# Performance work log

Measured on AMD Instinct MI355X. Metric: run time of the kernel, lower is better.

Reference implementation:

```python
import jax, jax.numpy as jnp
import numpy as np

NUM_NODES = 100000
NUM_EDGES = 500000
HID = 256


def setup_inputs() -> dict:
    key = jax.random.key(0)
    ks = jax.random.split(key, 6)
    emb_src = jax.random.normal(ks[0], (NUM_NODES, HID), dtype=jnp.float32)
    emb_dst = jax.random.normal(ks[1], (NUM_NODES, HID), dtype=jnp.float32)
    edge_label_index = jax.random.randint(ks[2], (2, NUM_EDGES), 0, NUM_NODES, dtype=jnp.int32)
    # torch Linear(2H, H) weight is [H, 2H]; we store transposed [2H, H] for x @ W
    W1 = jax.random.normal(ks[3], (2 * HID, HID), dtype=jnp.float32) * (1.0 / np.sqrt(2 * HID))
    b1 = jnp.zeros((HID,), dtype=jnp.float32)
    W2 = jax.random.normal(ks[4], (HID, 1), dtype=jnp.float32) * (1.0 / np.sqrt(HID))
    b2 = jnp.zeros((1,), dtype=jnp.float32)
    return {"emb_src": emb_src, "emb_dst": emb_dst, "edge_label_index": edge_label_index,
            "W1": W1, "b1": b1, "W2": W2, "b2": b2}


def reference(emb_src, emb_dst, edge_label_index, W1, b1, W2, b2):
    # decode(): gather src/dst embeddings, concat, Linear-ReLU-Linear, squeeze
    src_idx = edge_label_index[0]
    dst_idx = edge_label_index[1]
    h_src = emb_src[src_idx]          # [E, H] irregular gather
    h_dst = emb_dst[dst_idx]          # [E, H]
    # concat([h_src, h_dst]) @ W1 == h_src @ W1[:H] + h_dst @ W1[H:]
    # (avoids materializing the [E, 2H] concatenated tensor)
    h = jnp.dot(h_src, W1[:HID]) + jnp.dot(h_dst, W1[HID:]) + b1  # [E, H]
    h = jax.nn.relu(h)
    logits = (jnp.dot(h, W2) + b2)[:, 0]  # [E]
    return logits
```

## Files before the change

kernel.cpp:

```cpp
#include <hip/hip_runtime.h>
#include <hip/hip_bf16.h>
#include <stdint.h>

#define HID 256
#define BM  64
#define LDA 68
#define LDC 264

typedef __bf16 bf16x8 __attribute__((ext_vector_type(8)));
typedef float  f32x4  __attribute__((ext_vector_type(4)));

__device__ __forceinline__ ushort f2bf(float x) {
    union { float f; uint32_t u; } v; v.f = x;
    uint32_t u = v.u;
    uint32_t r = u + 0x7fffu + ((u >> 16) & 1u);
    return (ushort)(r >> 16);
}

__device__ __forceinline__ uint32_t pack2bf(float a, float b) {
    union { float f; uint32_t u; } ua, ub;
    ua.f = a; ub.f = b;
    return __builtin_amdgcn_perm(ub.u + 0x8000u, ua.u + 0x8000u, 0x07060302u);
}

__device__ __forceinline__ float uaf(uint32_t x) {
    union { uint32_t u; float f; } c; c.u = x; return c.f;
}

__global__ void conv_w1(const float* __restrict__ W1, ushort* __restrict__ Wt4) {
    __shared__ ushort tr[32][33];
    const int bk = blockIdx.x >> 3;
    const int bn = blockIdx.x & 7;
    const int t  = threadIdx.x;
    #pragma unroll
    for (int i = 0; i < 4; ++i) {
        int e = t + 256 * i; int r = e >> 5, cc = e & 31;
        tr[cc][r] = f2bf(W1[(size_t)(bk * 32 + r) * HID + bn * 32 + cc]);
    }
    __syncthreads();
    #pragma unroll
    for (int i = 0; i < 4; ++i) {
        int e = t + 256 * i; int rn = e >> 5, ck = e & 31;
        int k = bk * 32 + ck;
        int grp = k >> 3;
        int j   = k & 7;
        int n   = bn * 32 + rn;
        Wt4[((size_t)grp * HID + n) * 8 + j] = tr[rn][ck];
    }
}

__global__ __launch_bounds__(256, 4)
void node_gemm(const float* __restrict__ emb0, const float* __restrict__ emb1,
               const ushort* __restrict__ Wt4,
               ushort* __restrict__ u0, ushort* __restrict__ u1,
               int n0, int n1, int nb0) {
    __shared__ __align__(16) union {
        ushort As[4][BM * LDA];
        ushort Cs[32 * LDC];
    } sm;

    const int t    = threadIdx.x;
    const int tb   = (blockIdx.x >= nb0) ? 1 : 0;
    const int bloc = blockIdx.x - tb * nb0;
    const float*  emb = tb ? emb1 : emb0;
    ushort*       uo  = tb ? u1 : u0;
    const int     n   = tb ? n1 : n0;
    const int     e0  = bloc * BM;

    const int wave = t >> 6, lane = t & 63, q = lane >> 4, cl = lane & 15;

    const int r0  = t >> 4, seg = t & 15;
    int rcl[4];
    #pragma unroll
    for (int i = 0; i < 4; ++i) {
        int r = e0 + r0 + 16 * i; if (r > n - 1) r = n - 1;
        rcl[i] = r;
    }
    const float* abase = emb + seg * 4;
    const int    sbase = r0 * LDA + seg * 4;

    {
        float4 g[4][4];
        #pragma unroll
        for (int c = 0; c < 4; ++c)
            #pragma unroll
            for (int i = 0; i < 4; ++i)
                g[c][i] = *reinterpret_cast<const float4*>(
                    abase + (size_t)rcl[i] * HID + c * 64);
        #pragma unroll
        for (int c = 0; c < 4; ++c)
            #pragma unroll
            for (int i = 0; i < 4; ++i) {
                uint2 v;
                v.x = pack2bf(g[c][i].x, g[c][i].y);
                v.y = pack2bf(g[c][i].z, g[c][i].w);
                *reinterpret_cast<uint2*>(&sm.As[c][sbase + i * 16 * LDA]) = v;
            }
    }
    __syncthreads();

    f32x4 acc[4][4] = {};

    #pragma unroll 1
    for (int c = 0; c < 4; ++c) {
        bf16x8 bfr[2][4];
        #pragma unroll
        for (int ks = 0; ks < 2; ++ks) {
            const ushort* bb = Wt4 + ((size_t)(tb * 32 + c * 8 + ks * 4 + q) * HID) * 8;
            #pragma unroll
            for (int ni = 0; ni < 4; ++ni)
                bfr[ks][ni] = *reinterpret_cast<const bf16x8*>(
                    bb + (wave * 64 + ni * 16 + cl) * 8);
        }
        #pragma unroll
        for (int ks = 0; ks < 2; ++ks) {
            bf16x8 af[4];
            #pragma unroll
            for (int mi = 0; mi < 4; ++mi)
                af[mi] = *reinterpret_cast<const bf16x8*>(
                    &sm.As[c][(mi * 16 + cl) * LDA + ks * 32 + q * 8]);
            #pragma unroll
            for (int mi = 0; mi < 4; ++mi)
                #pragma unroll
                for (int ni = 0; ni < 4; ++ni)
                    acc[mi][ni] = __builtin_amdgcn_mfma_f32_16x16x32_bf16(
                        af[mi], bfr[ks][ni], acc[mi][ni], 0, 0, 0);
        }
    }

    __syncthreads();

    #pragma unroll
    for (int h = 0; h < 2; ++h) {
        #pragma unroll
        for (int mh = 0; mh < 2; ++mh) {
            const int mi = h * 2 + mh;
            #pragma unroll
            for (int ni = 0; ni < 4; ++ni)
                #pragma unroll
                for (int r = 0; r < 4; ++r)
                    sm.Cs[(mh * 16 + q * 4 + r) * LDC + wave * 64 + ni * 16 + cl] =
                        f2bf(acc[mi][ni][r]);
        }
        __syncthreads();

        #pragma unroll
        for (int i = 0; i < 4; ++i) {
            int f = t + 256 * i;
            int row = f >> 5, unit = f & 31;
            int grow = e0 + h * 32 + row;
            if (grow < n) {
                uint4 w = *reinterpret_cast<const uint4*>(&sm.Cs[row * LDC + unit * 8]);
                *reinterpret_cast<uint4*>(uo + (size_t)grow * HID + unit * 8) = w;
            }
        }
        if (h == 0) __syncthreads();
    }
}

#define EB 8
__global__ __launch_bounds__(256, 4)
void lp_edge(const ushort* __restrict__ u, const ushort* __restrict__ v,
             const int* __restrict__ eli,
             const float* __restrict__ b1, const float* __restrict__ W2,
             const float* __restrict__ b2, float* __restrict__ out,
             int E, int nwaves) {
    const int lane = threadIdx.x & 63;
    const int half = lane >> 5, sub = lane & 31;
    const int wid  = blockIdx.x * (blockDim.x >> 6) + (threadIdx.x >> 6);

    float b1v[8], w2v[8];
    {
        const float4* p1 = reinterpret_cast<const float4*>(b1 + sub * 8);
        const float4* p2 = reinterpret_cast<const float4*>(W2 + sub * 8);
        float4 a = p1[0], b = p1[1], c = p2[0], d = p2[1];
        b1v[0]=a.x; b1v[1]=a.y; b1v[2]=a.z; b1v[3]=a.w;
        b1v[4]=b.x; b1v[5]=b.y; b1v[6]=b.z; b1v[7]=b.w;
        w2v[0]=c.x; w2v[1]=c.y; w2v[2]=c.z; w2v[3]=c.w;
        w2v[4]=d.x; w2v[5]=d.y; w2v[6]=d.z; w2v[7]=d.w;
    }
    const float bias2 = b2[0];
    const ushort* tab  = half ? v : u;
    const int*    idxp = eli + (size_t)half * E;

    auto gather = [&](int b, uint4* gg) {
        #pragma unroll
        for (int j = 0; j < EB; ++j) {
            int e = b + j; if (e > E - 1) e = E - 1;
            int row = idxp[e];
            gg[j] = *reinterpret_cast<const uint4*>(tab + (size_t)row * HID + sub * 8);
        }
    };
    auto process = [&](const uint4* gg, int b) {
        float res = 0.f;
        #pragma unroll
        for (int j = 0; j < EB; ++j) {
            uint32_t pd[4], gd[4] = { gg[j].x, gg[j].y, gg[j].z, gg[j].w };
            #pragma unroll
            for (int c = 0; c < 4; ++c) pd[c] = (uint32_t)__shfl_xor((int)gd[c], 32);
            float acc = 0.f;
            #pragma unroll
            for (int c = 0; c < 4; ++c) {
                float a0 = uaf(gd[c] << 16), a1 = uaf(gd[c] & 0xffff0000u);
                float o0 = uaf(pd[c] << 16), o1 = uaf(pd[c] & 0xffff0000u);
                float h0 = fmaxf(a0 + o0 + b1v[2 * c], 0.f);
                float h1 = fmaxf(a1 + o1 + b1v[2 * c + 1], 0.f);
                acc = fmaf(h0, w2v[2 * c], acc);
                acc = fmaf(h1, w2v[2 * c + 1], acc);
            }
            #pragma unroll
            for (int m = 1; m <= 16; m <<= 1) acc += __shfl_xor(acc, m);
            if (half == 0 && sub == j) res = acc + bias2;
        }
        int e = b + sub;
        if (half == 0 && sub < EB && e < E) out[e] = res;
    };

    const int step = nwaves * EB;
    int base = wid * EB;
    uint4 gA[EB], gB[EB];
    gather(base, gA);
    while (base < E) {
        gather(base + step, gB);
        process(gA, base);
        base += step;
        if (base >= E) break;
        gather(base + step, gA);
        process(gB, base);
        base += step;
    }
}

__global__ __launch_bounds__(256, 3)
void lp_mono(const float* __restrict__ es, const float* __restrict__ ed,
             const int* __restrict__ eli, const float* __restrict__ W1,
             const float* __restrict__ b1, const float* __restrict__ W2,
             const float* __restrict__ b2,
             float* __restrict__ out, int E) {
    __shared__ __align__(16) ushort As[2][BM * LDA];
    __shared__ int   sIdx[2][BM];
    __shared__ float hred[4][BM];

    const int t = threadIdx.x, e0 = blockIdx.x * BM;
    const int wave = t >> 6, lane = t & 63, q = lane >> 4, cl = lane & 15;

    if (t < 2 * BM) {
        int which = t >> 6, e = t & 63;
        int ge = e0 + e; if (ge > E - 1) ge = E - 1;
        sIdx[which][e] = eli[which * E + ge];
    }
    __syncthreads();

    int ge_[2], go_[2], rsrc[2], rdst[2];
    #pragma unroll
    for (int i = 0; i < 2; ++i) {
        int c2 = t + 256 * i;
        ge_[i] = c2 >> 3; go_[i] = c2 & 7;
        rsrc[i] = sIdx[0][ge_[i]];
        rdst[i] = sIdx[1][ge_[i]];
    }
    float4 g0[2], g1[2];
    auto gather = [&](int c) {
        const float* tab = (c < 4) ? es : ed;
        #pragma unroll
        for (int i = 0; i < 2; ++i) {
            int row = (c < 4) ? rsrc[i] : rdst[i];
            const float* p = tab + (size_t)row * HID + (c & 3) * 64 + go_[i] * 8;
            g0[i] = *reinterpret_cast<const float4*>(p);
            g1[i] = *reinterpret_cast<const float4*>(p + 4);
        }
    };
    auto cvstore = [&](int buf) {
        #pragma unroll
        for (int i = 0; i < 2; ++i) {
            uint4 v;
            v.x = pack2bf(g0[i].x, g0[i].y); v.y = pack2bf(g0[i].z, g0[i].w);
            v.z = pack2bf(g1[i].x, g1[i].y); v.w = pack2bf(g1[i].z, g1[i].w);
            *reinterpret_cast<uint4*>(&As[buf][ge_[i] * LDA + go_[i] * 8]) = v;
        }
    };
    gather(0); cvstore(0); __syncthreads();
    f32x4 acc[4][4] = {};
    #pragma unroll
    for (int c = 0; c < 8; ++c) {
        const int cur = c & 1;
        if (c < 7) gather(c + 1);
        #pragma unroll
        for (int ks = 0; ks < 2; ++ks) {
            bf16x8 af[4], bfr[4];
            #pragma unroll
            for (int mi = 0; mi < 4; ++mi)
                af[mi] = *reinterpret_cast<const bf16x8*>(
                    &As[cur][(mi * 16 + cl) * LDA + ks * 32 + q * 8]);
            #pragma unroll
            for (int ni = 0; ni < 4; ++ni) {
                int nn = wave * 64 + ni * 16 + cl;
                union { ushort s[8]; bf16x8 v; } u;
                #pragma unroll
                for (int j = 0; j < 8; ++j)
                    u.s[j] = f2bf(W1[(size_t)(c * 64 + ks * 32 + q * 8 + j) * HID + nn]);
                bfr[ni] = u.v;
            }
            #pragma unroll
            for (int mi = 0; mi < 4; ++mi)
                #pragma unroll
                for (int ni = 0; ni < 4; ++ni)
                    acc[mi][ni] = __builtin_amdgcn_mfma_f32_16x16x32_bf16(
                        af[mi], bfr[ni], acc[mi][ni], 0, 0, 0);
        }
        if (c < 7) { cvstore(cur ^ 1); __syncthreads(); }
    }
    float b1v[4], w2v[4];
    #pragma unroll
    for (int ni = 0; ni < 4; ++ni) {
        int col = wave * 64 + ni * 16 + cl;
        b1v[ni] = b1[col]; w2v[ni] = W2[col];
    }
    #pragma unroll
    for (int mi = 0; mi < 4; ++mi) {
        #pragma unroll
        for (int r = 0; r < 4; ++r) {
            float s = 0.f;
            #pragma unroll
            for (int ni = 0; ni < 4; ++ni) {
                float h = acc[mi][ni][r] + b1v[ni];
                h = fmaxf(h, 0.f);
                s += h * w2v[ni];
            }
            s += __shfl_xor(s, 1); s += __shfl_xor(s, 2);
            s += __shfl_xor(s, 4); s += __shfl_xor(s, 8);
            if (cl == 0) hred[wave][mi * 16 + q * 4 + r] = s;
        }
    }
    __syncthreads();
    if (t < BM) {
        int ge = e0 + t;
        if (ge < E)
            out[ge] = hred[0][t] + hred[1][t] + hred[2][t] + hred[3][t] + b2[0];
    }
}

extern "C" void kernel_launch(void* const* d_in, const int* in_sizes, int n_in,
                              void* d_out, int out_size, void* d_ws, size_t ws_size,
                              hipStream_t stream) {
    const float* emb_src = (const float*)d_in[0];
    const float* emb_dst = (const float*)d_in[1];
    const int*   eli     = (const int*)d_in[2];
    const float* W1      = (const float*)d_in[3];
    const float* b1      = (const float*)d_in[4];
    const float* W2      = (const float*)d_in[5];
    const float* b2      = (const float*)d_in[6];
    float*       out     = (float*)d_out;

    const int E   = in_sizes[2] / 2;
    const int n0n = in_sizes[0] / HID;
    const int n1n = in_sizes[1] / HID;

    const size_t wtB = (size_t)2 * HID * 2 * HID * sizeof(ushort);
    const size_t uB  = (size_t)n0n * HID * sizeof(ushort);
    const size_t vB  = (size_t)n1n * HID * sizeof(ushort);

    ushort* Wt4 = (ushort*)d_ws;
    ushort* u0  = (ushort*)((char*)d_ws + wtB);
    ushort* u1  = (ushort*)((char*)d_ws + wtB + uB);

    const int fullPath = ws_size >= wtB + uB + vB;

    if (fullPath) {
        conv_w1<<<128, 256, 0, stream>>>(W1, Wt4);
        const int nb0 = (n0n + BM - 1) / BM;
        const int nb1 = (n1n + BM - 1) / BM;
        node_gemm<<<nb0 + nb1, 256, 0, stream>>>(emb_src, emb_dst, Wt4,
                                                 u0, u1, n0n, n1n, nb0);
        const int eb = 2048;
        lp_edge<<<eb, 256, 0, stream>>>(u0, u1, eli, b1, W2, b2, out, E, eb * 4);
    } else {
        const int nb = (E + BM - 1) / BM;
        lp_mono<<<nb, 256, 0, stream>>>(emb_src, emb_dst, eli, W1,
                                        b1, W2, b2, out, E);
    }
}
```

Baseline: 324.9 us.

## Make node GEMM persistent with double-buffered prefetch of embedding chunks

Turns node_gemm into a persistent kernel on a grid of at most 1024 blocks that loops over tiles. It double-buffers the A tile in LDS by K-chunk, prefetching the next chunk (or the next tile's first chunk) into registers while the MFMAs run on the current one. The LDS-staged coalesced output store is replaced with direct scattered 2-byte global stores from the accumulators. This shrinks shared memory use, but adds a barrier per chunk, uncoalesced output writes and a lower launch-bounds occupancy hint.

```diff
diff --git a/kernel.cpp b/kernel.cpp
--- a/kernel.cpp
+++ b/kernel.cpp
@@ -49,112 +49,132 @@
     }
 }
 
-__global__ __launch_bounds__(256, 4)
+__global__ __launch_bounds__(256, 3)
 void node_gemm(const float* __restrict__ emb0, const float* __restrict__ emb1,
                const ushort* __restrict__ Wt4,
                ushort* __restrict__ u0, ushort* __restrict__ u1,
-               int n0, int n1, int nb0) {
-    __shared__ __align__(16) union {
-        ushort As[4][BM * LDA];
-        ushort Cs[32 * LDC];
-    } sm;
+               int n0, int n1, int nb0, int ntiles) {
+    __shared__ __align__(16) ushort As[2][BM * LDA];
 
     const int t    = threadIdx.x;
-    const int tb   = (blockIdx.x >= nb0) ? 1 : 0;
-    const int bloc = blockIdx.x - tb * nb0;
-    const float*  emb = tb ? emb1 : emb0;
-    ushort*       uo  = tb ? u1 : u0;
-    const int     n   = tb ? n1 : n0;
-    const int     e0  = bloc * BM;
-
     const int wave = t >> 6, lane = t & 63, q = lane >> 4, cl = lane & 15;
-
-    const int r0  = t >> 4, seg = t & 15;
-    int rcl[4];
+    const int r0   = t >> 4, seg = t & 15;
+    const int sbase = r0 * LDA + seg * 4;
+
+    int tile = blockIdx.x;
+    if (tile >= ntiles) return;
+
+    int tbA = (tile >= nb0) ? 1 : 0;
+    const float* embA = tbA ? emb1 : emb0;
+    ushort*      uoA  = tbA ? u1 : u0;
+    int nA  = tbA ? n1 : n0;
+    int e0A = (tile - tbA * nb0) * BM;
+    int rclA[4];
     #pragma unroll
     for (int i = 0; i < 4; ++i) {
-        int r = e0 + r0 + 16 * i; if (r > n - 1) r = n - 1;
-        rcl[i] = r;
-    }
-    const float* abase = emb + seg * 4;
-    const int    sbase = r0 * LDA + seg * 4;
-
-    {
-        float4 g[4][4];
-        #pragma unroll
-        for (int c = 0; c < 4; ++c)
-            #pragma unroll
-            for (int i = 0; i < 4; ++i)
-                g[c][i] = *reinterpret_cast<const float4*>(
-                    abase + (size_t)rcl[i] * HID + c * 64);
-        #pragma unroll
-        for (int c = 0; c < 4; ++c)
+        int r = e0A + r0 + 16 * i; if (r > nA - 1) r = nA - 1;
+        rclA[i] = r;
+    }
+
+    float4 g[4];
+    auto cvstore = [&](int buf) {
+        #pragma unroll
+        for (int i = 0; i < 4; ++i) {
+            uint2 v;
+            v.x = pack2bf(g[i].x, g[i].y);
+            v.y = pack2bf(g[i].z, g[i].w);
+            *reinterpret_cast<uint2*>(&As[buf][sbase + i * 16 * LDA]) = v;
+        }
+    };
+
+    #pragma unroll
+    for (int i = 0; i < 4; ++i)
+        g[i] = *reinterpret_cast<const float4*>(embA + (size_t)rclA[i] * HID + seg * 4);
+    cvstore(0);
+    __syncthreads();
+    int cur = 0;
+
+    while (true) {
+        const int  tileNext = tile + gridDim.x;
+        const bool hasNext  = tileNext < ntiles;
+
+        int tbB = 0, nB = 0, e0B = 0;
+        const float* embB = embA; ushort* uoB = uoA;
+        int rclB[4];
+        if (hasNext) {
+            tbB  = (tileNext >= nb0) ? 1 : 0;
+            embB = tbB ? emb1 : emb0;
+            uoB  = tbB ? u1 : u0;
+            nB   = tbB ? n1 : n0;
+            e0B  = (tileNext - tbB * nb0) * BM;
             #pragma unroll
             for (int i = 0; i < 4; ++i) {
-                uint2 v;
-                v.x = pack2bf(g[c][i].x, g[c][i].y);
-                v.y = pack2bf(g[c][i].z, g[c][i].w);
-                *reinterpret_cast<uint2*>(&sm.As[c][sbase + i * 16 * LDA]) = v;
-            }
-    }
-    __syncthreads();
-
-    f32x4 acc[4][4] = {};
-
-    #pragma unroll 1
-    for (int c = 0; c < 4; ++c) {
-        bf16x8 bfr[2][4];
-        #pragma unroll
-        for (int ks = 0; ks < 2; ++ks) {
-            const ushort* bb = Wt4 + ((size_t)(tb * 32 + c * 8 + ks * 4 + q) * HID) * 8;
-            #pragma unroll
-            for (int ni = 0; ni < 4; ++ni)
-                bfr[ks][ni] = *reinterpret_cast<const bf16x8*>(
-                    bb + (wave * 64 + ni * 16 + cl) * 8);
-        }
-        #pragma unroll
-        for (int ks = 0; ks < 2; ++ks) {
-            bf16x8 af[4];
-            #pragma unroll
-            for (int mi = 0; mi < 4; ++mi)
-                af[mi] = *reinterpret_cast<const bf16x8*>(
-                    &sm.As[c][(mi * 16 + cl) * LDA + ks * 32 + q * 8]);
-            #pragma unroll
-            for (int mi = 0; mi < 4; ++mi)
+                int r = e0B + r0 + 16 * i; if (r > nB - 1) r = nB - 1;
+                rclB[i] = r;
+            }
+        }
+
+        f32x4 acc[4][4] = {};
+
+        #pragma unroll
+        for (int c = 0; c < 4; ++c) {
+            bf16x8 bfr[2][4];
+            #pragma unroll
+            for (int ks = 0; ks < 2; ++ks) {
+                const ushort* bb = Wt4 + ((size_t)(tbA * 32 + c * 8 + ks * 4 + q) * HID) * 8;
                 #pragma unroll
                 for (int ni = 0; ni < 4; ++ni)
-                    acc[mi][ni] = __builtin_amdgcn_mfma_f32_16x16x32_bf16(
-                        af[mi], bfr[ks][ni], acc[mi][ni], 0, 0, 0);
-        }
-    }
-
-    __syncthreads();
-
-    #pragma unroll
-    for (int h = 0; h < 2; ++h) {
-        #pragma unroll
-        for (int mh = 0; mh < 2; ++mh) {
-            const int mi = h * 2 + mh;
-            #pragma unroll
-            for (int ni = 0; ni < 4; ++ni)
-                #pragma unroll
-                for (int r = 0; r < 4; ++r)
-                    sm.Cs[(mh * 16 + q * 4 + r) * LDC + wave * 64 + ni * 16 + cl] =
-                        f2bf(acc[mi][ni][r]);
-        }
-        __syncthreads();
-
-        #pragma unroll
-        for (int i = 0; i < 4; ++i) {
-            int f = t + 256 * i;
-            int row = f >> 5, unit = f & 31;
-            int grow = e0 + h * 32 + row;
-            if (grow < n) {
-                uint4 w = *reinterpret_cast<const uint4*>(&sm.Cs[row * LDC + unit * 8]);
-                *reinterpret_cast<uint4*>(uo + (size_t)grow * HID + unit * 8) = w;
-            }
-        }
-        if (h == 0) __syncthreads();
+                    bfr[ks][ni] = *reinterpret_cast<const bf16x8*>(
+                        bb + (wave * 64 + ni * 16 + cl) * 8);
+            }
+            if (c < 3) {
+                #pragma unroll
+                for (int i = 0; i < 4; ++i)
+                    g[i] = *reinterpret_cast<const float4*>(
+                        embA + (size_t)rclA[i] * HID + seg * 4 + (c + 1) * 64);
+            } else if (hasNext) {
+                #pragma unroll
+                for (int i = 0; i < 4; ++i)
+                    g[i] = *reinterpret_cast<const float4*>(
+                        embB + (size_t)rclB[i] * HID + seg * 4);
+            }
+            #pragma unroll
+            for (int ks = 0; ks < 2; ++ks) {
+                #pragma unroll
+                for (int mi = 0; mi < 4; ++mi) {
+                    bf16x8 af = *reinterpret_cast<const bf16x8*>(
+                        &As[cur][(mi * 16 + cl) * LDA + ks * 32 + q * 8]);
+                    #pragma unroll
+                    for (int ni = 0; ni < 4; ++ni)
+                        acc[mi][ni] = __builtin_amdgcn_mfma_f32_16x16x32_bf16(
+                            af, bfr[ks][ni], acc[mi][ni], 0, 0, 0);
+                }
+            }
+            if (c < 3 || hasNext) {
+                cvstore(cur ^ 1);
+                __syncthreads();
+                cur ^= 1;
+            }
+        }
+
+        #pragma unroll
+        for (int mi = 0; mi < 4; ++mi)
+            #pragma unroll
+            for (int r_ = 0; r_ < 4; ++r_) {
+                int row = e0A + mi * 16 + q * 4 + r_;
+                if (row < nA) {
+                    ushort* up = uoA + (size_t)row * HID + wave * 64 + cl;
+                    #pragma unroll
+                    for (int ni = 0; ni < 4; ++ni)
+                        up[ni * 16] = f2bf(acc[mi][ni][r_]);
+                }
+            }
+
+        if (!hasNext) break;
+        tile = tileNext;
+        tbA = tbB; embA = embB; uoA = uoB; nA = nB; e0A = e0B;
+        #pragma unroll
+        for (int i = 0; i < 4; ++i) rclA[i] = rclB[i];
     }
 }
 
@@ -370,8 +390,10 @@
         conv_w1<<<128, 256, 0, stream>>>(W1, Wt4);
         const int nb0 = (n0n + BM - 1) / BM;
         const int nb1 = (n1n + BM - 1) / BM;
-        node_gemm<<<nb0 + nb1, 256, 0, stream>>>(emb_src, emb_dst, Wt4,
-                                                 u0, u1, n0n, n1n, nb0);
+        const int ntiles = nb0 + nb1;
+        int ngrid = ntiles < 1024 ? ntiles : 1024;
+        node_gemm<<<ngrid, 256, 0, stream>>>(emb_src, emb_dst, Wt4,
+                                             u0, u1, n0n, n1n, nb0, ntiles);
         const int eb = 2048;
         lp_edge<<<eb, 256, 0, stream>>>(u0, u1, eli, b1, W2, b2, out, E, eb * 4);
     } else {
```

After: 365.1 us. +12.4%, slower.

## Double-buffer A tile chunks in node_gemm to overlap global loads with MFMA

Applied to the files above, without the earlier changes.

Replaces the up-front load of all four K-chunks of the embedding tile into LDS with a two-buffer software pipeline. The next chunk's global loads and bf16 conversion now overlap with MFMA work on the current chunk, using a custom barrier that waits only on LDS counters. LDS use is halved, but the launch-bounds occupancy hint drops from 4 to 3 waves per SIMD, which may cost latency hiding across blocks.

```diff
diff --git a/kernel.cpp b/kernel.cpp
--- a/kernel.cpp
+++ b/kernel.cpp
@@ -25,6 +25,13 @@
 
 __device__ __forceinline__ float uaf(uint32_t x) {
     union { uint32_t u; float f; } c; c.u = x; return c.f;
+}
+
+__device__ __forceinline__ void wavebar() {
+    asm volatile("s_waitcnt lgkmcnt(0)" ::: "memory");
+    __builtin_amdgcn_sched_barrier(0);
+    __builtin_amdgcn_s_barrier();
+    __builtin_amdgcn_sched_barrier(0);
 }
 
 __global__ void conv_w1(const float* __restrict__ W1, ushort* __restrict__ Wt4) {
@@ -49,13 +56,13 @@
     }
 }
 
-__global__ __launch_bounds__(256, 4)
+__global__ __launch_bounds__(256, 3)
 void node_gemm(const float* __restrict__ emb0, const float* __restrict__ emb1,
                const ushort* __restrict__ Wt4,
                ushort* __restrict__ u0, ushort* __restrict__ u1,
                int n0, int n1, int nb0) {
     __shared__ __align__(16) union {
-        ushort As[4][BM * LDA];
+        ushort As[2][BM * LDA];
         ushort Cs[32 * LDC];
     } sm;
 
@@ -79,31 +86,25 @@
     const float* abase = emb + seg * 4;
     const int    sbase = r0 * LDA + seg * 4;
 
-    {
-        float4 g[4][4];
-        #pragma unroll
-        for (int c = 0; c < 4; ++c)
-            #pragma unroll
-            for (int i = 0; i < 4; ++i)
-                g[c][i] = *reinterpret_cast<const float4*>(
-                    abase + (size_t)rcl[i] * HID + c * 64);
-        #pragma unroll
-        for (int c = 0; c < 4; ++c)
-            #pragma unroll
-            for (int i = 0; i < 4; ++i) {
-                uint2 v;
-                v.x = pack2bf(g[c][i].x, g[c][i].y);
-                v.y = pack2bf(g[c][i].z, g[c][i].w);
-                *reinterpret_cast<uint2*>(&sm.As[c][sbase + i * 16 * LDA]) = v;
-            }
-    }
-    __syncthreads();
+    float4 ga[4], gb[4];
+    auto gload = [&](float4* g, int c) {
+        #pragma unroll
+        for (int i = 0; i < 4; ++i)
+            g[i] = *reinterpret_cast<const float4*>(abase + (size_t)rcl[i] * HID + c * 64);
+    };
+    auto cvst = [&](const float4* g, int buf) {
+        #pragma unroll
+        for (int i = 0; i < 4; ++i) {
+            uint2 v;
+            v.x = pack2bf(g[i].x, g[i].y);
+            v.y = pack2bf(g[i].z, g[i].w);
+            *reinterpret_cast<uint2*>(&sm.As[buf][sbase + i * 16 * LDA]) = v;
+        }
+    };
 
     f32x4 acc[4][4] = {};
-
-    #pragma unroll 1
-    for (int c = 0; c < 4; ++c) {
-        bf16x8 bfr[2][4];
+    bf16x8 bfr[2][4];
+    auto bload = [&](int c) {
         #pragma unroll
         for (int ks = 0; ks < 2; ++ks) {
             const ushort* bb = Wt4 + ((size_t)(tb * 32 + c * 8 + ks * 4 + q) * HID) * 8;
@@ -112,21 +113,41 @@
                 bfr[ks][ni] = *reinterpret_cast<const bf16x8*>(
                     bb + (wave * 64 + ni * 16 + cl) * 8);
         }
+    };
+    auto mm = [&](int buf) {
         #pragma unroll
         for (int ks = 0; ks < 2; ++ks) {
-            bf16x8 af[4];
-            #pragma unroll
-            for (int mi = 0; mi < 4; ++mi)
-                af[mi] = *reinterpret_cast<const bf16x8*>(
-                    &sm.As[c][(mi * 16 + cl) * LDA + ks * 32 + q * 8]);
-            #pragma unroll
-            for (int mi = 0; mi < 4; ++mi)
+            #pragma unroll
+            for (int mi = 0; mi < 4; ++mi) {
+                bf16x8 af = *reinterpret_cast<const bf16x8*>(
+                    &sm.As[buf][(mi * 16 + cl) * LDA + ks * 32 + q * 8]);
                 #pragma unroll
                 for (int ni = 0; ni < 4; ++ni)
                     acc[mi][ni] = __builtin_amdgcn_mfma_f32_16x16x32_bf16(
-                        af[mi], bfr[ks][ni], acc[mi][ni], 0, 0, 0);
-        }
-    }
+                        af, bfr[ks][ni], acc[mi][ni], 0, 0, 0);
+            }
+        }
+    };
+
+    gload(ga, 0);
+    cvst(ga, 0);
+    gload(ga, 1);
+    wavebar();
+
+    bload(0); gload(gb, 2);
+    mm(0);
+    cvst(ga, 1);
+    wavebar();
+    bload(1); gload(ga, 3);
+    mm(1);
+    cvst(gb, 0);
+    wavebar();
+    bload(2);
+    mm(0);
+    cvst(ga, 1);
+    wavebar();
+    bload(3);
+    mm(1);
 
     __syncthreads();
 
```

After: 324.6 us. No clear change (-0.1%).

## Restructure node GEMM into per-wave 16-row tiles without block-level shared staging

Applied to the files above, without the earlier changes.

The node projection GEMM now has each wave own a 16-row tile across all 256 output columns. A fragments are loaded straight from global fp32 into registers and converted to bf16, and W fragments stream from global memory. This drops the block-wide shared-memory A staging and the __syncthreads barriers, and uses a private per-wave LDS buffer for the bf16 output transpose. In exchange, W1 is re-read per 16-row tile rather than per 64-row block, register pressure rises (launch bounds lowered to 3), and A rows are read with narrower, less coalesced accesses.

```diff
diff --git a/kernel.cpp b/kernel.cpp
--- a/kernel.cpp
+++ b/kernel.cpp
@@ -49,112 +49,64 @@
     }
 }
 
-__global__ __launch_bounds__(256, 4)
+__global__ __launch_bounds__(256, 3)
 void node_gemm(const float* __restrict__ emb0, const float* __restrict__ emb1,
                const ushort* __restrict__ Wt4,
                ushort* __restrict__ u0, ushort* __restrict__ u1,
-               int n0, int n1, int nb0) {
-    __shared__ __align__(16) union {
-        ushort As[4][BM * LDA];
-        ushort Cs[32 * LDC];
-    } sm;
-
-    const int t    = threadIdx.x;
-    const int tb   = (blockIdx.x >= nb0) ? 1 : 0;
-    const int bloc = blockIdx.x - tb * nb0;
-    const float*  emb = tb ? emb1 : emb0;
-    ushort*       uo  = tb ? u1 : u0;
-    const int     n   = tb ? n1 : n0;
-    const int     e0  = bloc * BM;
-
-    const int wave = t >> 6, lane = t & 63, q = lane >> 4, cl = lane & 15;
-
-    const int r0  = t >> 4, seg = t & 15;
-    int rcl[4];
-    #pragma unroll
-    for (int i = 0; i < 4; ++i) {
-        int r = e0 + r0 + 16 * i; if (r > n - 1) r = n - 1;
-        rcl[i] = r;
-    }
-    const float* abase = emb + seg * 4;
-    const int    sbase = r0 * LDA + seg * 4;
-
-    {
-        float4 g[4][4];
-        #pragma unroll
-        for (int c = 0; c < 4; ++c)
-            #pragma unroll
-            for (int i = 0; i < 4; ++i)
-                g[c][i] = *reinterpret_cast<const float4*>(
-                    abase + (size_t)rcl[i] * HID + c * 64);
-        #pragma unroll
-        for (int c = 0; c < 4; ++c)
-            #pragma unroll
-            for (int i = 0; i < 4; ++i) {
-                uint2 v;
-                v.x = pack2bf(g[c][i].x, g[c][i].y);
-                v.y = pack2bf(g[c][i].z, g[c][i].w);
-                *reinterpret_cast<uint2*>(&sm.As[c][sbase + i * 16 * LDA]) = v;
-            }
-    }
-    __syncthreads();
-
-    f32x4 acc[4][4] = {};
-
-    #pragma unroll 1
-    for (int c = 0; c < 4; ++c) {
-        bf16x8 bfr[2][4];
-        #pragma unroll
-        for (int ks = 0; ks < 2; ++ks) {
-            const ushort* bb = Wt4 + ((size_t)(tb * 32 + c * 8 + ks * 4 + q) * HID) * 8;
-            #pragma unroll
-            for (int ni = 0; ni < 4; ++ni)
-                bfr[ks][ni] = *reinterpret_cast<const bf16x8*>(
-                    bb + (wave * 64 + ni * 16 + cl) * 8);
-        }
-        #pragma unroll
-        for (int ks = 0; ks < 2; ++ks) {
-            bf16x8 af[4];
-            #pragma unroll
-            for (int mi = 0; mi < 4; ++mi)
-                af[mi] = *reinterpret_cast<const bf16x8*>(
-                    &sm.As[c][(mi * 16 + cl) * LDA + ks * 32 + q * 8]);
-            #pragma unroll
-            for (int mi = 0; mi < 4; ++mi)
-                #pragma unroll
-                for (int ni = 0; ni < 4; ++ni)
-                    acc[mi][ni] = __builtin_amdgcn_mfma_f32_16x16x32_bf16(
-                        af[mi], bfr[ks][ni], acc[mi][ni], 0, 0, 0);
-        }
-    }
-
-    __syncthreads();
-
-    #pragma unroll
-    for (int h = 0; h < 2; ++h) {
-        #pragma unroll
-        for (int mh = 0; mh < 2; ++mh) {
-            const int mi = h * 2 + mh;
-            #pragma unroll
-            for (int ni = 0; ni < 4; ++ni)
-                #pragma unroll
-                for (int r = 0; r < 4; ++r)
-                    sm.Cs[(mh * 16 + q * 4 + r) * LDC + wave * 64 + ni * 16 + cl] =
-                        f2bf(acc[mi][ni][r]);
-        }
-        __syncthreads();
-
-        #pragma unroll
-        for (int i = 0; i < 4; ++i) {
-            int f = t + 256 * i;
-            int row = f >> 5, unit = f & 31;
-            int grow = e0 + h * 32 + row;
-            if (grow < n) {
-                uint4 w = *reinterpret_cast<const uint4*>(&sm.Cs[row * LDC + unit * 8]);
-                *reinterpret_cast<uint4*>(uo + (size_t)grow * HID + unit * 8) = w;
-            }
-        }
-        if (h == 0) __syncthreads();
+               int n0, int n1, int nt0, int ntiles) {
+    __shared__ __align__(16) ushort Cw[4][16 * LDC];
+
+    const int wave = threadIdx.x >> 6, lane = threadIdx.x & 63;
+    const int q = lane >> 4, cl = lane & 15;
+    const int tile = blockIdx.x * 4 + wave;
+    if (tile >= ntiles) return;
+
+    const int tb  = (tile >= nt0) ? 1 : 0;
+    const float* emb = tb ? emb1 : emb0;
+    ushort*      uo  = tb ? u1 : u0;
+    const int    n   = tb ? n1 : n0;
+    const int    base = (tile - tb * nt0) * 16;
+
+    int arow = base + cl; if (arow > n - 1) arow = n - 1;
+    const float* ap = emb + (size_t)arow * HID + q * 8;
+
+    f32x4 acc[16] = {};
+
+    #pragma unroll
+    for (int c = 0; c < 8; ++c) {
+        const ushort* bb = Wt4 + ((size_t)(tb * 32 + c * 4 + q) * HID + cl) * 8;
+        bf16x8 bfr[16];
+        #pragma unroll
+        for (int ni = 0; ni < 16; ++ni)
+            bfr[ni] = *reinterpret_cast<const bf16x8*>(bb + ni * 16 * 8);
+        float4 a0 = *reinterpret_cast<const float4*>(ap + c * 32);
+        float4 a1 = *reinterpret_cast<const float4*>(ap + c * 32 + 4);
+        union { uint32_t u[4]; bf16x8 v; } af;
+        af.u[0] = pack2bf(a0.x, a0.y); af.u[1] = pack2bf(a0.z, a0.w);
+        af.u[2] = pack2bf(a1.x, a1.y); af.u[3] = pack2bf(a1.z, a1.w);
+        #pragma unroll
+        for (int ni = 0; ni < 16; ++ni)
+            acc[ni] = __builtin_amdgcn_mfma_f32_16x16x32_bf16(
+                af.v, bfr[ni], acc[ni], 0, 0, 0);
+    }
+
+    ushort* cw = Cw[wave];
+    #pragma unroll
+    for (int ni = 0; ni < 16; ++ni)
+        #pragma unroll
+        for (int r = 0; r < 4; ++r)
+            cw[(q * 4 + r) * LDC + ni * 16 + cl] = f2bf(acc[ni][r]);
+    asm volatile("s_waitcnt lgkmcnt(0)" ::: "memory");
+    __builtin_amdgcn_sched_barrier(0);
+    #pragma unroll
+    for (int i = 0; i < 8; ++i) {
+        int f = lane + 64 * i;
+        int row = f >> 5, unit = f & 31;
+        int grow = base + row;
+        if (grow < n) {
+            uint4 w = *reinterpret_cast<const uint4*>(&cw[row * LDC + unit * 8]);
+            *reinterpret_cast<uint4*>(uo + (size_t)grow * HID + unit * 8) = w;
+        }
     }
 }
 
@@ -368,10 +320,12 @@
 
     if (fullPath) {
         conv_w1<<<128, 256, 0, stream>>>(W1, Wt4);
-        const int nb0 = (n0n + BM - 1) / BM;
-        const int nb1 = (n1n + BM - 1) / BM;
-        node_gemm<<<nb0 + nb1, 256, 0, stream>>>(emb_src, emb_dst, Wt4,
-                                                 u0, u1, n0n, n1n, nb0);
+        const int nt0 = (n0n + 15) / 16;
+        const int nt1 = (n1n + 15) / 16;
+        const int ntiles = nt0 + nt1;
+        const int nblk = (ntiles + 3) / 4;
+        node_gemm<<<nblk, 256, 0, stream>>>(emb_src, emb_dst, Wt4,
+                                            u0, u1, n0n, n1n, nt0, ntiles);
         const int eb = 2048;
         lp_edge<<<eb, 256, 0, stream>>>(u0, u1, eli, b1, W2, b2, out, E, eb * 4);
     } else {
```

Result: slower. 368.8 us (+13.5%).
